# Kernel tuning notes

Measured on AMD Instinct MI355X. Metric: run time of the kernel, lower is better.

Reference implementation:

```python
import jax, jax.numpy as jnp
import numpy as np


def setup_inputs() -> dict:
    key = jax.random.key(0)
    kx, kw = jax.random.split(key)
    B, C, H = 32, 1024, 64
    x = jax.random.normal(kx, (B, C, H, H), dtype=jnp.float32)
    w = jax.random.normal(kw, (1, C), dtype=jnp.float32) * 0.02  # Linear(1024,1) weight
    b = jnp.zeros((1,), dtype=jnp.float32)                       # Linear bias
    mode = 0  # 0 == 'source' (label 0), 1 == 'target' (label 1)
    return {"x": x, "w": w, "b": b, "mode": mode}


def reference(x, w, b, mode):
    # fc1 applied at every spatial location: logits [B, H, W]
    logits = jnp.einsum('bchw,c->bhw', x, w[0]) + b[0]
    # Original applies Sigmoid, then BCEWithLogitsLoss (which sigmoids again).
    z = jax.nn.sigmoid(logits)
    y = jnp.asarray(mode, dtype=z.dtype)  # label: 0 for source, 1 for target
    # BCEWithLogits(z, y) = softplus(z) - z*y (stable since z in (0,1))
    per_elem = jax.nn.softplus(z) - z * y
    # sum over pixels of per-pixel batch mean, divided by H*W == global mean
    return jnp.mean(per_elem)
```

## Files before the change

### kernel.cpp

```cpp
#include <hip/hip_runtime.h>
#include <math.h>

constexpr int B_ = 32;
constexpr int C_ = 1024;
constexpr int HW = 64 * 64;
constexpr int NSPATIAL = B_ * HW;
constexpr int BLOCK = 256;
constexpr int TILE = 1024;
constexpr int NTILES = NSPATIAL / TILE;

__global__ __launch_bounds__(BLOCK) void k_dot(
    const float4* __restrict__ x4, const float* __restrict__ w,
    float4* __restrict__ part4, int cpc ) {
    __shared__ float ws[1024];
    const int tile  = blockIdx.x;
    const int chunk = blockIdx.y;
    const int c0    = chunk * cpc;
    const int t     = threadIdx.x;

    for (int c = t; c < cpc; c += BLOCK) ws[c] = w[c0 + c];
    __syncthreads();

    const int b   = tile >> 2;
    const int hw4 = (tile & 3) * (TILE / 4) + t;
    const float4* p = x4 + (size_t)(b * C_ + c0) * (HW / 4) + hw4;

    float4 acc = make_float4(0.f, 0.f, 0.f, 0.f);
    #pragma unroll 4
    for (int c = 0; c < cpc; ++c) {
        float4 v = p[(size_t)c * (HW / 4)];
        float wc = ws[c];
        acc.x += wc * v.x;
        acc.y += wc * v.y;
        acc.z += wc * v.z;
        acc.w += wc * v.w;
    }
    part4[(size_t)chunk * (NSPATIAL / 4) + (size_t)tile * (TILE / 4) + t] = acc;
}

__global__ __launch_bounds__(BLOCK) void k_finish(
    const float4* __restrict__ part4, const float* __restrict__ bias,
    const int* __restrict__ mode, float* __restrict__ blocksum, int nchunks) {
    const int t   = threadIdx.x;
    const int idx = blockIdx.x * BLOCK + t;

    float4 s = make_float4(0.f, 0.f, 0.f, 0.f);
    for (int k = 0; k < nchunks; ++k) {
        float4 v = part4[(size_t)k * (NSPATIAL / 4) + idx];
        s.x += v.x; s.y += v.y; s.z += v.z; s.w += v.w;
    }
    const float bb = bias[0];
    const float y  = (float)mode[0];

    float vals[4] = {s.x, s.y, s.z, s.w};
    float local = 0.f;
    #pragma unroll
    for (int j = 0; j < 4; ++j) {
        float logit = vals[j] + bb;
        float z  = 1.f / (1.f + __expf(-logit));
        float pe = log1pf(__expf(z)) - z * y;
        local += pe;
    }

    __shared__ float red[BLOCK];
    red[t] = local;
    __syncthreads();
    for (int off = BLOCK / 2; off > 0; off >>= 1) {
        if (t < off) red[t] += red[t + off];
        __syncthreads();
    }
    if (t == 0) blocksum[blockIdx.x] = red[0];
}

__global__ __launch_bounds__(128) void k_final(
    const float* __restrict__ blocksum, float* __restrict__ out) {
    __shared__ float red[128];
    const int t = threadIdx.x;
    red[t] = blocksum[t];
    __syncthreads();
    for (int off = 64; off > 0; off >>= 1) {
        if (t < off) red[t] += red[t + off];
        __syncthreads();
    }
    if (t == 0) out[0] = red[0] / (float)NSPATIAL;
}

extern "C" void kernel_launch(void* const* d_in, const int* in_sizes, int n_in,
                              void* d_out, int out_size, void* d_ws, size_t ws_size,
                              hipStream_t stream) {
    const float4* x4  = (const float4*)d_in[0];
    const float*  w   = (const float*)d_in[1];
    const float*  bia = (const float*)d_in[2];
    const int*    mod = (const int*)d_in[3];
    float* out = (float*)d_out;

    int nchunks = 8;
    while (nchunks > 1 &&
           (size_t)nchunks * NSPATIAL * sizeof(float) + 128 * sizeof(float) > ws_size)
        nchunks >>= 1;
    const int cpc = C_ / nchunks;

    float4* part4    = (float4*)d_ws;
    float*  blocksum = (float*)((char*)d_ws + (size_t)nchunks * NSPATIAL * sizeof(float));

    dim3 grid1(NTILES, nchunks);
    k_dot<<<grid1, BLOCK, 0, stream>>>(x4, w, part4, cpc);
    k_finish<<<NSPATIAL / 4 / BLOCK, BLOCK, 0, stream>>>(part4, bia, mod, blocksum, nchunks);
    k_final<<<1, 128, 0, stream>>>(blocksum, out);
}
```

Baseline: 101.3 us.

## Fuse channel-split dot product and loss into one kernel with in-block reduction

Replaces the grid-level channel chunking, which wrote partial logits to workspace before a separate finishing kernel, with one kernel. Each block's four wavefronts each cover a quarter of the channels for 256 pixels, combine their partials in shared memory, apply the sigmoid/softplus loss, and reduce with wave shuffles. This drops the partial-sum global round trip and one kernel launch. In exchange there are 512 blocks of 256 threads with only 64 independent loads in flight per thread, which may reduce memory-level parallelism on a bandwidth-bound 512MB read.

```diff
diff --git a/kernel.cpp b/kernel.cpp
--- a/kernel.cpp
+++ b/kernel.cpp
@@ -6,79 +6,75 @@
 constexpr int HW = 64 * 64;
 constexpr int NSPATIAL = B_ * HW;
 constexpr int BLOCK = 256;
-constexpr int TILE = 1024;
-constexpr int NTILES = NSPATIAL / TILE;
+constexpr int PX_PER_BLOCK = 256;
+constexpr int NBLOCKS = NSPATIAL / PX_PER_BLOCK;
 
-__global__ __launch_bounds__(BLOCK) void k_dot(
-    const float4* __restrict__ x4, const float* __restrict__ w,
-    float4* __restrict__ part4, int cpc ) {
-    __shared__ float ws[1024];
-    const int tile  = blockIdx.x;
-    const int chunk = blockIdx.y;
-    const int c0    = chunk * cpc;
-    const int t     = threadIdx.x;
+__global__ __launch_bounds__(BLOCK) void k_main(
+    const float4* __restrict__ x4, const float4* __restrict__ w4g,
+    const float* __restrict__ bias, const int* __restrict__ mode,
+    float* __restrict__ blocksum) {
+    __shared__ float4 w4[C_ / 4];
+    __shared__ float4 red[BLOCK];
 
-    for (int c = t; c < cpc; c += BLOCK) ws[c] = w[c0 + c];
+    const int t    = threadIdx.x;
+    const int wv   = t >> 6;
+    const int lane = t & 63;
+
+    w4[t] = w4g[t];
     __syncthreads();
 
-    const int b   = tile >> 2;
-    const int hw4 = (tile & 3) * (TILE / 4) + t;
-    const float4* p = x4 + (size_t)(b * C_ + c0) * (HW / 4) + hw4;
+    const int blk = blockIdx.x;
+    const int b   = blk >> 4;
+    const int hw4 = (blk & 15) * 64 + lane;
+
+    const float4* p = x4 + ((size_t)(b * C_ + wv * 256) * (HW / 4)) + hw4;
 
     float4 acc = make_float4(0.f, 0.f, 0.f, 0.f);
     #pragma unroll 4
-    for (int c = 0; c < cpc; ++c) {
-        float4 v = p[(size_t)c * (HW / 4)];
-        float wc = ws[c];
-        acc.x += wc * v.x;
-        acc.y += wc * v.y;
-        acc.z += wc * v.z;
-        acc.w += wc * v.w;
+    for (int kk = 0; kk < 64; ++kk) {
+        float4 wc = w4[wv * 64 + kk];
+        float4 v0 = p[(size_t)(4 * kk + 0) * (HW / 4)];
+        float4 v1 = p[(size_t)(4 * kk + 1) * (HW / 4)];
+        float4 v2 = p[(size_t)(4 * kk + 2) * (HW / 4)];
+        float4 v3 = p[(size_t)(4 * kk + 3) * (HW / 4)];
+        acc.x += wc.x * v0.x + wc.y * v1.x + wc.z * v2.x + wc.w * v3.x;
+        acc.y += wc.x * v0.y + wc.y * v1.y + wc.z * v2.y + wc.w * v3.y;
+        acc.z += wc.x * v0.z + wc.y * v1.z + wc.z * v2.z + wc.w * v3.z;
+        acc.w += wc.x * v0.w + wc.y * v1.w + wc.z * v2.w + wc.w * v3.w;
     }
-    part4[(size_t)chunk * (NSPATIAL / 4) + (size_t)tile * (TILE / 4) + t] = acc;
+
+    red[t] = acc;
+    __syncthreads();
+
+    if (t < 64) {
+        float4 a0 = red[t], a1 = red[t + 64], a2 = red[t + 128], a3 = red[t + 192];
+        const float bb = bias[0];
+        const float y  = (float)mode[0];
+        float logit[4] = {a0.x + a1.x + a2.x + a3.x,
+                          a0.y + a1.y + a2.y + a3.y,
+                          a0.z + a1.z + a2.z + a3.z,
+                          a0.w + a1.w + a2.w + a3.w};
+        float local = 0.f;
+        #pragma unroll
+        for (int j = 0; j < 4; ++j) {
+            float lg = logit[j] + bb;
+            float z  = 1.f / (1.f + __expf(-lg));
+            local   += log1pf(__expf(z)) - z * y;
+        }
+        #pragma unroll
+        for (int off = 32; off > 0; off >>= 1)
+            local += __shfl_down(local, off, 64);
+        if (lane == 0) blocksum[blk] = local;
+    }
 }
 
-__global__ __launch_bounds__(BLOCK) void k_finish(
-    const float4* __restrict__ part4, const float* __restrict__ bias,
-    const int* __restrict__ mode, float* __restrict__ blocksum, int nchunks) {
-    const int t   = threadIdx.x;
-    const int idx = blockIdx.x * BLOCK + t;
-
-    float4 s = make_float4(0.f, 0.f, 0.f, 0.f);
-    for (int k = 0; k < nchunks; ++k) {
-        float4 v = part4[(size_t)k * (NSPATIAL / 4) + idx];
-        s.x += v.x; s.y += v.y; s.z += v.z; s.w += v.w;
-    }
-    const float bb = bias[0];
-    const float y  = (float)mode[0];
-
-    float vals[4] = {s.x, s.y, s.z, s.w};
-    float local = 0.f;
-    #pragma unroll
-    for (int j = 0; j < 4; ++j) {
-        float logit = vals[j] + bb;
-        float z  = 1.f / (1.f + __expf(-logit));
-        float pe = log1pf(__expf(z)) - z * y;
-        local += pe;
-    }
-
-    __shared__ float red[BLOCK];
-    red[t] = local;
-    __syncthreads();
-    for (int off = BLOCK / 2; off > 0; off >>= 1) {
-        if (t < off) red[t] += red[t + off];
-        __syncthreads();
-    }
-    if (t == 0) blocksum[blockIdx.x] = red[0];
-}
-
-__global__ __launch_bounds__(128) void k_final(
+__global__ __launch_bounds__(512) void k_final(
     const float* __restrict__ blocksum, float* __restrict__ out) {
-    __shared__ float red[128];
+    __shared__ float red[512];
     const int t = threadIdx.x;
     red[t] = blocksum[t];
     __syncthreads();
-    for (int off = 64; off > 0; off >>= 1) {
+    for (int off = 256; off > 0; off >>= 1) {
         if (t < off) red[t] += red[t + off];
         __syncthreads();
     }
@@ -89,22 +85,13 @@
                               void* d_out, int out_size, void* d_ws, size_t ws_size,
                               hipStream_t stream) {
     const float4* x4  = (const float4*)d_in[0];
-    const float*  w   = (const float*)d_in[1];
+    const float4* w4g = (const float4*)d_in[1];
     const float*  bia = (const float*)d_in[2];
     const int*    mod = (const int*)d_in[3];
     float* out = (float*)d_out;
 
-    int nchunks = 8;
-    while (nchunks > 1 &&
-           (size_t)nchunks * NSPATIAL * sizeof(float) + 128 * sizeof(float) > ws_size)
-        nchunks >>= 1;
-    const int cpc = C_ / nchunks;
+    float* blocksum = (float*)d_ws;
 
-    float4* part4    = (float4*)d_ws;
-    float*  blocksum = (float*)((char*)d_ws + (size_t)nchunks * NSPATIAL * sizeof(float));
-
-    dim3 grid1(NTILES, nchunks);
-    k_dot<<<grid1, BLOCK, 0, stream>>>(x4, w, part4, cpc);
-    k_finish<<<NSPATIAL / 4 / BLOCK, BLOCK, 0, stream>>>(part4, bia, mod, blocksum, nchunks);
-    k_final<<<1, 128, 0, stream>>>(blocksum, out);
+    k_main<<<NBLOCKS, BLOCK, 0, stream>>>(x4, w4g, bia, mod, blocksum);
+    k_final<<<1, 512, 0, stream>>>(blocksum, out);
 }
```

Measured after the change: 97.35 us. 1.04x faster.
